# Performance work log

Measured on AMD Instinct MI355X. Metric: run time of the kernel, lower is better.

Reference implementation:

```python
import jax, jax.numpy as jnp
import numpy as np

N, D, H, DH, FF, NE, NNZ = 4096, 128, 2, 64, 256, 2048, 65536
EPS = 1e-5

def layer_norm(x, g, b):
    m = jnp.mean(x, axis=-1, keepdims=True)
    v = jnp.var(x, axis=-1, keepdims=True)
    return (x - m) / jnp.sqrt(v + EPS) * g + b

def setup_inputs() -> dict:
    key = jax.random.key(0)
    ks = jax.random.split(key, 24)
    s = 0.05
    node_idx = jax.random.randint(ks[1], (NNZ,), 0, N)
    he_idx = jax.random.randint(ks[2], (NNZ,), 0, NE)
    return {
        "x": jax.random.normal(ks[0], (N, D), dtype=jnp.float32),
        "edge": jnp.stack([node_idx, he_idx]).astype(jnp.int64),
        "Wq": jax.random.normal(ks[3], (D, D)) * s, "bq": jnp.zeros((D,)),
        "Wk": jax.random.normal(ks[4], (D, D)) * s, "bk": jnp.zeros((D,)),
        "Wv": jax.random.normal(ks[5], (D, D)) * s, "bv": jnp.zeros((D,)),
        "Wo": jax.random.normal(ks[6], (D, D)) * s, "bo": jnp.zeros((D,)),
        "g_ln1": jnp.ones((D,)), "b_ln1": jnp.zeros((D,)),
        "W1": jax.random.normal(ks[7], (D, FF)) * s, "bf1": jnp.zeros((FF,)),
        "W2": jax.random.normal(ks[8], (FF, D)) * s, "bf2": jnp.zeros((D,)),
        "g_ln2": jnp.ones((D,)), "b_ln2": jnp.zeros((D,)),
        "Wh": jax.random.normal(ks[9], (D, D)) * s, "bh": jnp.zeros((D,)),
    }

def reference(x, edge, Wq, bq, Wk, bk, Wv, bv, Wo, bo, g_ln1, b_ln1,
              W1, bf1, W2, bf2, g_ln2, b_ln2, Wh, bh):
    # dropout layers run in eval mode (identity) for a deterministic reference
    def mha_block(h):
        q = (h @ Wq + bq).reshape(N, H, DH)
        k = (h @ Wk + bk).reshape(N, H, DH)
        v = (h @ Wv + bv).reshape(N, H, DH)
        scores = jnp.einsum('nhd,mhd->hnm', q, k) / jnp.sqrt(jnp.float32(DH))
        attn = jax.nn.softmax(scores, axis=-1)            # [H,N,N]
        o = jnp.einsum('hnm,mhd->nhd', attn, v).reshape(N, D)
        return layer_norm(h + o @ Wo + bo, g_ln1, b_ln1)

    def ff_block(h):
        z = jax.nn.sigmoid(h @ W1 + bf1)
        return layer_norm(h + z @ W2 + bf2, g_ln2, b_ln2)

    h = ff_block(mha_block(x))
    h = ff_block(mha_block(h))

    # HypergraphConv: out = D^{-1} H B^{-1} H^T (X Theta) + bias
    node_idx = edge[0]
    he_idx = edge[1]
    xt = h @ Wh                                            # [N,D]
    ones = jnp.ones((NNZ,), dtype=xt.dtype)
    Bdeg = jax.ops.segment_sum(ones, he_idx, num_segments=NE)
    Binv = jnp.where(Bdeg > 0, 1.0 / Bdeg, 0.0)
    Ddeg = jax.ops.segment_sum(ones, node_idx, num_segments=N)
    Dinv = jnp.where(Ddeg > 0, 1.0 / Ddeg, 0.0)
    e = jax.ops.segment_sum(xt[node_idx], he_idx, num_segments=NE) * Binv[:, None]
    out = jax.ops.segment_sum(e[he_idx], node_idx, num_segments=N) * Dinv[:, None] + bh
    return jax.nn.relu(out)
```

## Files before the change

kernel.cpp:

```cpp
#include <hip/hip_runtime.h>
#include <hip/hip_bf16.h>
#include <cstddef>

#define N_NODES 4096
#define DIM     128
#define NHEAD   2
#define DHEAD   64
#define FFDIM   256
#define NEDGE   2048
#define NNZ_E   65536
#define NSPLIT  8

typedef __attribute__((ext_vector_type(8))) short bf16x8;
typedef __attribute__((ext_vector_type(4))) float f32x4;
typedef unsigned short u16;

__device__ __forceinline__ u16 f2b(float f) {
    unsigned u = __float_as_uint(f);
    return (u16)((u + 0x7FFFu + ((u >> 16) & 1u)) >> 16);
}
__device__ __forceinline__ float b2f_bits(u16 h) {
    return __uint_as_float(((unsigned)h) << 16);
}
__device__ __forceinline__ unsigned cvtpk(float a, float b) {
    unsigned r;
    asm("v_cvt_pk_bf16_f32 %0, %1, %2" : "=v"(r) : "v"(a), "v"(b));
    return r;
}

__global__ void prep(const float* __restrict__ x, float* __restrict__ h,
                     u16* __restrict__ hh, u16* __restrict__ hl,
                     const float* W0, const float* W1, const float* W2,
                     const float* W3, const float* W4, const float* W5,
                     const float* W6,
                     u16* P0, u16* P1, u16* P2, u16* P3, u16* P4, u16* P5, u16* P6,
                     const int* __restrict__ edge_raw,
                     int* __restrict__ nidx, int* __restrict__ hidx,
                     int* __restrict__ cnt_e, int* __restrict__ cnt_n) {
    const int bx = blockIdx.x;
    if (bx < 2048) {
        int i = bx * 256 + threadIdx.x;
        float f = x[i];
        h[i] = f;
        u16 hi = f2b(f);
        hh[i] = hi;
        hl[i] = f2b(f - b2f_bits(hi));
        return;
    }
    if (bx >= 2944) {
        __shared__ int is64_s;
        if (threadIdx.x < 64) {
            int v = edge_raw[2 * threadIdx.x + 1];
            unsigned long long bal = __ballot(v != 0);
            if (threadIdx.x == 0) is64_s = (bal == 0ull) ? 1 : 0;
        }
        __syncthreads();
        const int is64 = is64_s;
        int i = (bx - 2944) * 256 + threadIdx.x;
        if (i < NNZ_E) {
            int ni = (is64 ? edge_raw[2 * i]             : edge_raw[i])         & (N_NODES - 1);
            int he = (is64 ? edge_raw[2 * NNZ_E + 2 * i] : edge_raw[NNZ_E + i]) & (NEDGE - 1);
            nidx[i] = ni;
            hidx[i] = he;
            atomicAdd(&cnt_n[ni], 1);
            atomicAdd(&cnt_e[he], 1);
        }
        return;
    }
    const int p = bx - 2048;
    const int sel = p >> 7;
    const float* W; u16* P; int K, NC;
    switch (sel) {
        case 0: W = W0; P = P0; K = 128; NC = 128; break;
        case 1: W = W1; P = P1; K = 128; NC = 128; break;
        case 2: W = W2; P = P2; K = 128; NC = 128; break;
        case 3: W = W3; P = P3; K = 128; NC = 128; break;
        case 4: W = W4; P = P4; K = 128; NC = 128; break;
        case 5: W = W5; P = P5; K = 128; NC = 256; break;
        default: W = W6; P = P6; K = 256; NC = 128; break;
    }
    int i = (p & 127) * 256 + threadIdx.x;
    if (i < K * NC) {
        int k = i / NC, n = i % NC;
        float f = W[i];
        u16 hb = f2b(f);
        size_t o = ((size_t)(k >> 3) * NC + n) * 8 + (k & 7);
        P[o] = hb;
        P[(size_t)K * NC + o] = f2b(f - b2f_bits(hb));
    }
}

__global__ __launch_bounds__(256) void qkv_mfma(const u16* __restrict__ Ah,
                                                const u16* __restrict__ Al,
                                                const u16* __restrict__ Wq,
                                                const u16* __restrict__ Wk,
                                                const u16* __restrict__ Wv,
                                                const float* __restrict__ bq,
                                                const float* __restrict__ bk,
                                                const float* __restrict__ bv,
                                                u16* __restrict__ qb,
                                                u16* __restrict__ kb,
                                                u16* __restrict__ vtb) {
    const int K = 128, NC = 128;
    const int tid = threadIdx.x, w = tid >> 6, lane = tid & 63;
    const int qi = lane & 15, gi = lane >> 4;
    const int row0 = blockIdx.x * 64 + w * 16;
    const int sel = blockIdx.y >> 2;
    const int col0 = (blockIdx.y & 3) * 32;
    const u16* Wp = (sel == 0) ? Wq : (sel == 1) ? Wk : Wv;
    const float* bias = (sel == 0) ? bq : (sel == 1) ? bk : bv;
    const u16* Wlo = Wp + (size_t)K * NC;

    f32x4 acc[2];
    acc[0] = (f32x4){0.f, 0.f, 0.f, 0.f};
    acc[1] = (f32x4){0.f, 0.f, 0.f, 0.f};

#pragma unroll 4
    for (int kc = 0; kc < K / 32; ++kc) {
        const int k0 = kc * 32;
        const size_t ao = (size_t)(row0 + qi) * K + k0 + gi * 8;
        bf16x8 ah = *(const bf16x8*)(Ah + ao);
        bf16x8 al = *(const bf16x8*)(Al + ao);
#pragma unroll
        for (int c = 0; c < 2; ++c) {
            const size_t wo = ((size_t)(k0 / 8 + gi) * NC + col0 + c * 16 + qi) * 8;
            bf16x8 wh = *(const bf16x8*)(Wp + wo);
            bf16x8 wl = *(const bf16x8*)(Wlo + wo);
            acc[c] = __builtin_amdgcn_mfma_f32_16x16x32_bf16(ah, wh, acc[c], 0, 0, 0);
            acc[c] = __builtin_amdgcn_mfma_f32_16x16x32_bf16(al, wh, acc[c], 0, 0, 0);
            acc[c] = __builtin_amdgcn_mfma_f32_16x16x32_bf16(ah, wl, acc[c], 0, 0, 0);
        }
    }

#pragma unroll
    for (int c = 0; c < 2; ++c) {
        const int col = col0 + c * 16 + qi;
        const int hh = col >> 6, d = col & 63;
        float bv_ = bias[col];
        if (sel < 2) {
            u16* dst = (sel == 0) ? qb : kb;
#pragma unroll
            for (int r = 0; r < 4; ++r) {
                const int grow = row0 + gi * 4 + r;
                dst[((size_t)hh * N_NODES + grow) * 64 + d] = f2b(acc[c][r] + bv_);
            }
        } else {
            const int grow0 = row0 + gi * 4;
            uint2 pw;
            pw.x = cvtpk(acc[c][0] + bv_, acc[c][1] + bv_);
            pw.y = cvtpk(acc[c][2] + bv_, acc[c][3] + bv_);
            *(uint2*)&vtb[((size_t)hh * 64 + d) * N_NODES + grow0] = pw;
        }
    }
}

#define ROWP 72
__global__ __launch_bounds__(256) void attn_mfma(const u16* __restrict__ qb,
                                                 const u16* __restrict__ kb,
                                                 const u16* __restrict__ vtb,
                                                 float* __restrict__ op,
                                                 float* __restrict__ mlm,
                                                 float* __restrict__ mll) {
    __shared__ __align__(16) u16 k_s[64 * ROWP];
    __shared__ __align__(16) u16 vt_s[64 * ROWP];
    __shared__ __align__(16) u16 p_s[4][16 * ROWP];
    const int h = blockIdx.y;
    const int s = blockIdx.z;
    const int row0 = blockIdx.x * 64;
    const int tid = threadIdx.x;
    const int w = tid >> 6, lane = tid & 63;
    const int qi = lane & 15, gi = lane >> 4;
    const float CE = 0.18033688011f;
    const float THR = 44.36f;

    const u16* qrow = qb + ((size_t)h * N_NODES + row0 + w * 16 + qi) * 64 + gi * 8;
    bf16x8 qf0 = *(const bf16x8*)qrow;
    bf16x8 qf1 = *(const bf16x8*)(qrow + 32);

    f32x4 oc[4];
#pragma unroll
    for (int i = 0; i < 4; ++i) oc[i] = (f32x4){0.f, 0.f, 0.f, 0.f};
    float m_run = -INFINITY, l_run = 0.f;

    const u16* kbh = kb + (size_t)h * N_NODES * 64;
    const u16* vth = vtb + (size_t)h * 64 * N_NODES;

    for (int kt = s * (N_NODES / 64 / NSPLIT); kt < (s + 1) * (N_NODES / 64 / NSPLIT); ++kt) {
        const u16* ksrc = kbh + kt * 64 * 64;
#pragma unroll
        for (int i = 0; i < 2; ++i) {
            int c = tid + i * 256;
            int r = c >> 3, ss = c & 7;
            *(uint4*)&k_s[r * ROWP + ss * 8]  = *(const uint4*)(ksrc + c * 8);
            *(uint4*)&vt_s[r * ROWP + ss * 8] = *(const uint4*)(vth + (size_t)r * N_NODES + kt * 64 + ss * 8);
        }
        __syncthreads();

        f32x4 sc[4];
#pragma unroll
        for (int t = 0; t < 4; ++t) {
            const u16* krow = &k_s[(t * 16 + qi) * ROWP + gi * 8];
            bf16x8 ka0 = *(const bf16x8*)krow;
            bf16x8 ka1 = *(const bf16x8*)(krow + 32);
            f32x4 z = (f32x4){0.f, 0.f, 0.f, 0.f};
            z = __builtin_amdgcn_mfma_f32_16x16x32_bf16(ka0, qf0, z, 0, 0, 0);
            sc[t] = __builtin_amdgcn_mfma_f32_16x16x32_bf16(ka1, qf1, z, 0, 0, 0);
        }

        float smax = -INFINITY;
#pragma unroll
        for (int t = 0; t < 4; ++t)
            smax = fmaxf(smax, fmaxf(fmaxf(sc[t][0], sc[t][1]), fmaxf(sc[t][2], sc[t][3])));
        smax = fmaxf(smax, __shfl_xor(smax, 16));
        smax = fmaxf(smax, __shfl_xor(smax, 32));

        const bool renew = !__all(smax <= m_run + THR);
        float alpha;
        if (renew) {
            float mn = fmaxf(m_run, smax);
            alpha = exp2f((m_run - mn) * CE);
            m_run = mn;
        }
        float nb = m_run * CE;
        float psum = 0.f;
#pragma unroll
        for (int t = 0; t < 4; ++t) {
            float p0 = exp2f(fmaf(sc[t][0], CE, -nb));
            float p1 = exp2f(fmaf(sc[t][1], CE, -nb));
            float p2 = exp2f(fmaf(sc[t][2], CE, -nb));
            float p3 = exp2f(fmaf(sc[t][3], CE, -nb));
            psum += (p0 + p1) + (p2 + p3);
            uint2 pw;
            pw.x = cvtpk(p0, p1);
            pw.y = cvtpk(p2, p3);
            *(uint2*)&p_s[w][qi * ROWP + t * 16 + gi * 4] = pw;
        }
        psum += __shfl_xor(psum, 16);
        psum += __shfl_xor(psum, 32);

        if (renew) {
            float a0 = __shfl(alpha, gi * 4 + 0);
            float a1 = __shfl(alpha, gi * 4 + 1);
            float a2 = __shfl(alpha, gi * 4 + 2);
            float a3 = __shfl(alpha, gi * 4 + 3);
#pragma unroll
            for (int d = 0; d < 4; ++d) {
                oc[d][0] *= a0; oc[d][1] *= a1; oc[d][2] *= a2; oc[d][3] *= a3;
            }
            l_run = l_run * alpha + psum;
        } else {
            l_run += psum;
        }

        const u16* prow = &p_s[w][qi * ROWP];
        bf16x8 pa0 = *(const bf16x8*)(prow + gi * 8);
        bf16x8 pa1 = *(const bf16x8*)(prow + 32 + gi * 8);
#pragma unroll
        for (int d = 0; d < 4; ++d) {
            const u16* vrow = &vt_s[(d * 16 + qi) * ROWP + gi * 8];
            bf16x8 vb0 = *(const bf16x8*)vrow;
            bf16x8 vb1 = *(const bf16x8*)(vrow + 32);
            oc[d] = __builtin_amdgcn_mfma_f32_16x16x32_bf16(pa0, vb0, oc[d], 0, 0, 0);
            oc[d] = __builtin_amdgcn_mfma_f32_16x16x32_bf16(pa1, vb1, oc[d], 0, 0, 0);
        }
        __syncthreads();
    }

    float* opd = op + (size_t)s * N_NODES * 128;
#pragma unroll
    for (int d = 0; d < 4; ++d) {
        size_t cb = h * 64 + d * 16 + qi;
        opd[(size_t)(row0 + w * 16 + gi * 4 + 0) * 128 + cb] = oc[d][0];
        opd[(size_t)(row0 + w * 16 + gi * 4 + 1) * 128 + cb] = oc[d][1];
        opd[(size_t)(row0 + w * 16 + gi * 4 + 2) * 128 + cb] = oc[d][2];
        opd[(size_t)(row0 + w * 16 + gi * 4 + 3) * 128 + cb] = oc[d][3];
    }
    if (gi == 0) {
        size_t mi = (size_t)s * NHEAD * N_NODES + (size_t)h * N_NODES + row0 + w * 16 + qi;
        mlm[mi] = m_run;
        mll[mi] = l_run;
    }
}

#define ROWA 136
#define ROWZ 264
#define ROWH 132
template<int DO_QKV>
__global__ __launch_bounds__(256) void mega_layer(
        const float* __restrict__ op, const float* __restrict__ mlm,
        const float* __restrict__ mll,
        const u16* __restrict__ wp_o, const float* __restrict__ bo,
        float* __restrict__ h,
        const float* __restrict__ g1, const float* __restrict__ b1,
        const u16* __restrict__ wp_1, const float* __restrict__ bf1,
        const u16* __restrict__ wp_2, const float* __restrict__ bf2,
        const float* __restrict__ g2, const float* __restrict__ b2,
        const u16* __restrict__ wp_q, const u16* __restrict__ wp_k,
        const u16* __restrict__ wp_v,
        const float* __restrict__ bq, const float* __restrict__ bk,
        const float* __restrict__ bv,
        u16* __restrict__ qb, u16* __restrict__ kb, u16* __restrict__ vtb,
        const u16* __restrict__ wp_h, float* __restrict__ xt) {
    __shared__ __align__(16) u16 zbuf[16 * ROWZ * 2];
    __shared__ __align__(16) u16 hp_hi[16 * ROWA];
    __shared__ __align__(16) u16 hp_lo[16 * ROWA];
    __shared__ float hln[16 * ROWH];
    __shared__ float ws_s[NSPLIT][32];
    __shared__ float Linv_s[32];
    __shared__ float wsum[4][16], wsq[4][16];
    const float CE = 0.18033688011f;
    const int tid = threadIdx.x, w = tid >> 6, lane = tid & 63;
    const int qi = lane & 15, gi = lane >> 4;
    const int row0 = blockIdx.x * 16;
    u16* a_hi = zbuf;
    u16* a_lo = zbuf + 16 * ROWA;
    u16* z_hi = zbuf;
    u16* z_lo = zbuf + 16 * ROWZ;

    if (tid < 32) {
        int r = tid >> 1, hd = tid & 1;
        size_t mb = (size_t)hd * N_NODES + row0 + r;
        float m[NSPLIT], l[NSPLIT], mx = -INFINITY;
#pragma unroll
        for (int s = 0; s < NSPLIT; ++s) {
            m[s] = mlm[mb + (size_t)s * NHEAD * N_NODES];
            l[s] = mll[mb + (size_t)s * NHEAD * N_NODES];
            mx = fmaxf(mx, m[s]);
        }
        float L = 0.f;
#pragma unroll
        for (int s = 0; s < NSPLIT; ++s) {
            float ws = exp2f((m[s] - mx) * CE);
            ws_s[s][tid] = ws;
            L += ws * l[s];
        }
        Linv_s[tid] = 1.f / L;
    }
    __syncthreads();

    for (int e = tid; e < 16 * 128; e += 256) {
        int r = e >> 7, c = e & 127, hd = c >> 6;
        size_t idx = (size_t)(row0 + r) * 128 + c;
        float O = 0.f;
#pragma unroll
        for (int s = 0; s < NSPLIT; ++s)
            O += ws_s[s][r * 2 + hd] * op[(size_t)s * N_NODES * 128 + idx];
        float v = O * Linv_s[r * 2 + hd];
        u16 hi = f2b(v);
        a_hi[r * ROWA + c] = hi;
        a_lo[r * ROWA + c] = f2b(v - b2f_bits(hi));
    }
    __syncthreads();

    {
        const u16* Wlo = wp_o + (size_t)128 * 128;
        f32x4 acc[2];
        acc[0] = (f32x4){0.f, 0.f, 0.f, 0.f};
        acc[1] = (f32x4){0.f, 0.f, 0.f, 0.f};
        const int col0 = w * 32;
#pragma unroll
        for (int kc = 0; kc < 4; ++kc) {
            const int k0 = kc * 32;
            bf16x8 ah = *(const bf16x8*)&a_hi[qi * ROWA + k0 + gi * 8];
            bf16x8 al = *(const bf16x8*)&a_lo[qi * ROWA + k0 + gi * 8];
#pragma unroll
            for (int c = 0; c < 2; ++c) {
                const size_t wo = ((size_t)(k0 / 8 + gi) * 128 + col0 + c * 16 + qi) * 8;
                bf16x8 wh = *(const bf16x8*)(wp_o + wo);
                bf16x8 wl = *(const bf16x8*)(Wlo + wo);
                acc[c] = __builtin_amdgcn_mfma_f32_16x16x32_bf16(ah, wh, acc[c], 0, 0, 0);
                acc[c] = __builtin_amdgcn_mfma_f32_16x16x32_bf16(al, wh, acc[c], 0, 0, 0);
                acc[c] = __builtin_amdgcn_mfma_f32_16x16x32_bf16(ah, wl, acc[c], 0, 0, 0);
            }
        }
        float y[2][4], rs[4], rq[4];
#pragma unroll
        for (int r = 0; r < 4; ++r) { rs[r] = 0.f; rq[r] = 0.f; }
#pragma unroll
        for (int c = 0; c < 2; ++c) {
            const int col = col0 + c * 16 + qi;
            float bv = bo[col];
#pragma unroll
            for (int r = 0; r < 4; ++r) {
                float v = acc[c][r] + bv + h[(size_t)(row0 + gi * 4 + r) * 128 + col];
                y[c][r] = v;
                rs[r] += v; rq[r] += v * v;
            }
        }
#pragma unroll
        for (int r = 0; r < 4; ++r)
            for (int msk = 1; msk < 16; msk <<= 1) {
                rs[r] += __shfl_xor(rs[r], msk);
                rq[r] += __shfl_xor(rq[r], msk);
            }
        if (qi == 0) {
#pragma unroll
            for (int r = 0; r < 4; ++r) { wsum[w][gi * 4 + r] = rs[r]; wsq[w][gi * 4 + r] = rq[r]; }
        }
        __syncthreads();
#pragma unroll
        for (int r = 0; r < 4; ++r) {
            const int lr = gi * 4 + r;
            float ts = wsum[0][lr] + wsum[1][lr] + wsum[2][lr] + wsum[3][lr];
            float tq = wsq[0][lr] + wsq[1][lr] + wsq[2][lr] + wsq[3][lr];
            float mean = ts * (1.f / 128.f);
            float var  = tq * (1.f / 128.f) - mean * mean;
            float rstd = rsqrtf(var + 1e-5f);
#pragma unroll
            for (int c = 0; c < 2; ++c) {
                const int col = col0 + c * 16 + qi;
                float yn = (y[c][r] - mean) * rstd * g1[col] + b1[col];
                hln[lr * ROWH + col] = yn;
                u16 hi = f2b(yn);
                hp_hi[lr * ROWA + col] = hi;
                hp_lo[lr * ROWA + col] = f2b(yn - b2f_bits(hi));
            }
        }
    }
    __syncthreads();

    {
        const u16* W1lo = wp_1 + (size_t)128 * 256;
        f32x4 acc1[4];
#pragma unroll
        for (int t = 0; t < 4; ++t) acc1[t] = (f32x4){0.f, 0.f, 0.f, 0.f};
#pragma unroll
        for (int kc = 0; kc < 4; ++kc) {
            const int k0 = kc * 32;
            bf16x8 ah = *(const bf16x8*)&hp_hi[qi * ROWA + k0 + gi * 8];
            bf16x8 al = *(const bf16x8*)&hp_lo[qi * ROWA + k0 + gi * 8];
#pragma unroll
            for (int t = 0; t < 4; ++t) {
                const size_t wo = ((size_t)(k0 / 8 + gi) * 256 + w * 64 + t * 16 + qi) * 8;
                bf16x8 wh = *(const bf16x8*)(wp_1 + wo);
                bf16x8 wl = *(const bf16x8*)(W1lo + wo);
                acc1[t] = __builtin_amdgcn_mfma_f32_16x16x32_bf16(ah, wh, acc1[t], 0, 0, 0);
                acc1[t] = __builtin_amdgcn_mfma_f32_16x16x32_bf16(al, wh, acc1[t], 0, 0, 0);
                acc1[t] = __builtin_amdgcn_mfma_f32_16x16x32_bf16(ah, wl, acc1[t], 0, 0, 0);
            }
        }
        __syncthreads();
#pragma unroll
        for (int t = 0; t < 4; ++t) {
            const int col = w * 64 + t * 16 + qi;
            float bv = bf1[col];
#pragma unroll
            for (int r = 0; r < 4; ++r) {
                float v = acc1[t][r] + bv;
                v = 1.f / (1.f + __expf(-v));
                u16 hi = f2b(v);
                const int zr = gi * 4 + r;
                z_hi[zr * ROWZ + col] = hi;
                z_lo[zr * ROWZ + col] = f2b(v - b2f_bits(hi));
            }
        }
    }
    __syncthreads();

    {
        const u16* W2lo = wp_2 + (size_t)256 * 128;
        f32x4 acc[2];
        acc[0] = (f32x4){0.f, 0.f, 0.f, 0.f};
        acc[1] = (f32x4){0.f, 0.f, 0.f, 0.f};
        const int col0 = w * 32;
#pragma unroll
        for (int kc = 0; kc < 8; ++kc) {
            const int k0 = kc * 32;
            bf16x8 ah = *(const bf16x8*)&z_hi[qi * ROWZ + k0 + gi * 8];
            bf16x8 al = *(const bf16x8*)&z_lo[qi * ROWZ + k0 + gi * 8];
#pragma unroll
            for (int c = 0; c < 2; ++c) {
                const size_t wo = ((size_t)(k0 / 8 + gi) * 128 + col0 + c * 16 + qi) * 8;
                bf16x8 wh = *(const bf16x8*)(wp_2 + wo);
                bf16x8 wl = *(const bf16x8*)(W2lo + wo);
                acc[c] = __builtin_amdgcn_mfma_f32_16x16x32_bf16(ah, wh, acc[c], 0, 0, 0);
                acc[c] = __builtin_amdgcn_mfma_f32_16x16x32_bf16(al, wh, acc[c], 0, 0, 0);
                acc[c] = __builtin_amdgcn_mfma_f32_16x16x32_bf16(ah, wl, acc[c], 0, 0, 0);
            }
        }
        float y[2][4], rs[4], rq[4];
#pragma unroll
        for (int r = 0; r < 4; ++r) { rs[r] = 0.f; rq[r] = 0.f; }
#pragma unroll
        for (int c = 0; c < 2; ++c) {
            const int col = col0 + c * 16 + qi;
            float bv = bf2[col];
#pragma unroll
            for (int r = 0; r < 4; ++r) {
                float v = acc[c][r] + bv + hln[(gi * 4 + r) * ROWH + col];
                y[c][r] = v;
                rs[r] += v; rq[r] += v * v;
            }
        }
#pragma unroll
        for (int r = 0; r < 4; ++r)
            for (int msk = 1; msk < 16; msk <<= 1) {
                rs[r] += __shfl_xor(rs[r], msk);
                rq[r] += __shfl_xor(rq[r], msk);
            }
        if (qi == 0) {
#pragma unroll
            for (int r = 0; r < 4; ++r) { wsum[w][gi * 4 + r] = rs[r]; wsq[w][gi * 4 + r] = rq[r]; }
        }
        __syncthreads();
#pragma unroll
        for (int r = 0; r < 4; ++r) {
            const int lr = gi * 4 + r;
            float ts = wsum[0][lr] + wsum[1][lr] + wsum[2][lr] + wsum[3][lr];
            float tq = wsq[0][lr] + wsq[1][lr] + wsq[2][lr] + wsq[3][lr];
            float mean = ts * (1.f / 128.f);
            float var  = tq * (1.f / 128.f) - mean * mean;
            float rstd = rsqrtf(var + 1e-5f);
#pragma unroll
            for (int c = 0; c < 2; ++c) {
                const int col = col0 + c * 16 + qi;
                float yn = (y[c][r] - mean) * rstd * g2[col] + b2[col];
                if (DO_QKV) h[(size_t)(row0 + lr) * 128 + col] = yn;
                u16 hi = f2b(yn);
                hp_hi[lr * ROWA + col] = hi;
                hp_lo[lr * ROWA + col] = f2b(yn - b2f_bits(hi));
            }
        }
    }

    if (DO_QKV) {
        __syncthreads();
        const int col0 = w * 32;
#pragma unroll
        for (int sel = 0; sel < 3; ++sel) {
            const u16* Wp = (sel == 0) ? wp_q : (sel == 1) ? wp_k : wp_v;
            const float* bias = (sel == 0) ? bq : (sel == 1) ? bk : bv;
            const u16* Wlo = Wp + (size_t)128 * 128;
            f32x4 acc[2];
            acc[0] = (f32x4){0.f, 0.f, 0.f, 0.f};
            acc[1] = (f32x4){0.f, 0.f, 0.f, 0.f};
#pragma unroll
            for (int kc = 0; kc < 4; ++kc) {
                const int k0 = kc * 32;
                bf16x8 ah = *(const bf16x8*)&hp_hi[qi * ROWA + k0 + gi * 8];
                bf16x8 al = *(const bf16x8*)&hp_lo[qi * ROWA + k0 + gi * 8];
#pragma unroll
                for (int c = 0; c < 2; ++c) {
                    const size_t wo = ((size_t)(k0 / 8 + gi) * 128 + col0 + c * 16 + qi) * 8;
                    bf16x8 wh = *(const bf16x8*)(Wp + wo);
                    bf16x8 wl = *(const bf16x8*)(Wlo + wo);
                    acc[c] = __builtin_amdgcn_mfma_f32_16x16x32_bf16(ah, wh, acc[c], 0, 0, 0);
                    acc[c] = __builtin_amdgcn_mfma_f32_16x16x32_bf16(al, wh, acc[c], 0, 0, 0);
                    acc[c] = __builtin_amdgcn_mfma_f32_16x16x32_bf16(ah, wl, acc[c], 0, 0, 0);
                }
            }
#pragma unroll
            for (int c = 0; c < 2; ++c) {
                const int col = col0 + c * 16 + qi;
                const int hh = col >> 6, d = col & 63;
                float bv_ = bias[col];
                if (sel < 2) {
                    u16* dst = (sel == 0) ? qb : kb;
#pragma unroll
                    for (int r = 0; r < 4; ++r) {
                        const int grow = row0 + gi * 4 + r;
                        dst[((size_t)hh * N_NODES + grow) * 64 + d] = f2b(acc[c][r] + bv_);
                    }
                } else {
                    const int grow0 = row0 + gi * 4;
                    uint2 pw;
                    pw.x = cvtpk(acc[c][0] + bv_, acc[c][1] + bv_);
                    pw.y = cvtpk(acc[c][2] + bv_, acc[c][3] + bv_);
                    *(uint2*)&vtb[((size_t)hh * 64 + d) * N_NODES + grow0] = pw;
                }
            }
        }
    } else {
        __syncthreads();
        const u16* Wlo = wp_h + (size_t)128 * 128;
        f32x4 acc[2];
        acc[0] = (f32x4){0.f, 0.f, 0.f, 0.f};
        acc[1] = (f32x4){0.f, 0.f, 0.f, 0.f};
        const int col0 = w * 32;
#pragma unroll
        for (int kc = 0; kc < 4; ++kc) {
            const int k0 = kc * 32;
            bf16x8 ah = *(const bf16x8*)&hp_hi[qi * ROWA + k0 + gi * 8];
            bf16x8 al = *(const bf16x8*)&hp_lo[qi * ROWA + k0 + gi * 8];
#pragma unroll
            for (int c = 0; c < 2; ++c) {
                const size_t wo = ((size_t)(k0 / 8 + gi) * 128 + col0 + c * 16 + qi) * 8;
                bf16x8 wh = *(const bf16x8*)(wp_h + wo);
                bf16x8 wl = *(const bf16x8*)(Wlo + wo);
                acc[c] = __builtin_amdgcn_mfma_f32_16x16x32_bf16(ah, wh, acc[c], 0, 0, 0);
                acc[c] = __builtin_amdgcn_mfma_f32_16x16x32_bf16(al, wh, acc[c], 0, 0, 0);
                acc[c] = __builtin_amdgcn_mfma_f32_16x16x32_bf16(ah, wl, acc[c], 0, 0, 0);
            }
        }
#pragma unroll
        for (int c = 0; c < 2; ++c) {
            const int col = col0 + c * 16 + qi;
#pragma unroll
            for (int r = 0; r < 4; ++r)
                xt[(size_t)(row0 + gi * 4 + r) * 128 + col] = acc[c][r];
        }
    }
}

__global__ __launch_bounds__(1024) void scan_only(const int* __restrict__ cnt_e,
                                                  const int* __restrict__ cnt_n,
                                                  int* __restrict__ off_e,
                                                  int* __restrict__ off_n,
                                                  int* __restrict__ cur_e,
                                                  int* __restrict__ cur_n) {
    __shared__ int s[N_NODES];
    const int he_side = (blockIdx.x == 0);
    const int n = he_side ? NEDGE : N_NODES;
    const int* cnt = he_side ? cnt_e : cnt_n;
    int* off = he_side ? off_e : off_n;
    int* cur = he_side ? cur_e : cur_n;
    for (int i = threadIdx.x; i < n; i += 1024) s[i] = cnt[i];
    __syncthreads();
    for (int st = 1; st < n; st <<= 1) {
        int v[4]; int nj = 0;
        for (int i = threadIdx.x; i < n; i += 1024) v[nj++] = (i >= st) ? s[i - st] : 0;
        __syncthreads();
        nj = 0;
        for (int i = threadIdx.x; i < n; i += 1024) s[i] += v[nj++];
        __syncthreads();
    }
    for (int i = threadIdx.x; i < n; i += 1024) { off[i + 1] = s[i]; cur[i] = 0; }
    if (threadIdx.x == 0) off[0] = 0;
}

__global__ void fill_csr(const int* __restrict__ nidx, const int* __restrict__ hidx,
                         const int* __restrict__ off_e, const int* __restrict__ off_n,
                         int* __restrict__ cur_e, int* __restrict__ cur_n,
                         int* __restrict__ csr_e, int* __restrict__ csr_n) {
    int i = blockIdx.x * 256 + threadIdx.x;
    if (i < NNZ_E) {
        int ni = nidx[i], he = hidx[i];
        int p = atomicAdd(&cur_e[he], 1);
        csr_e[off_e[he] + p] = ni;
        int q = atomicAdd(&cur_n[ni], 1);
        csr_n[off_n[ni] + q] = he;
    }
}

__global__ __launch_bounds__(128) void gather_e(const int* __restrict__ off_e,
                                                const int* __restrict__ csr_e,
                                                const float* __restrict__ xt,
                                                float* __restrict__ e_sc) {
    __shared__ int ms[128];
    const int he = blockIdx.x, d = threadIdx.x;
    const int beg = off_e[he], end = off_e[he + 1];
    float a0 = 0.f, a1 = 0.f, a2 = 0.f, a3 = 0.f;
    for (int c = beg; c < end; c += 128) {
        int nl = min(128, end - c);
        if (d < nl) ms[d] = csr_e[c + d];
        __syncthreads();
        int j = 0;
        for (; j + 3 < nl; j += 4) {
            a0 += xt[(size_t)ms[j]     * 128 + d];
            a1 += xt[(size_t)ms[j + 1] * 128 + d];
            a2 += xt[(size_t)ms[j + 2] * 128 + d];
            a3 += xt[(size_t)ms[j + 3] * 128 + d];
        }
        for (; j < nl; ++j) a0 += xt[(size_t)ms[j] * 128 + d];
        __syncthreads();
    }
    float binv = (end > beg) ? 1.f / (float)(end - beg) : 0.f;
    e_sc[(size_t)he * 128 + d] = ((a0 + a1) + (a2 + a3)) * binv;
}

__global__ __launch_bounds__(128) void gather_n(const int* __restrict__ off_n,
                                                const int* __restrict__ csr_n,
                                                const float* __restrict__ e_sc,
                                                const float* __restrict__ bh,
                                                float* __restrict__ out) {
    __shared__ int ms[128];
    const int nn = blockIdx.x, d = threadIdx.x;
    const int beg = off_n[nn], end = off_n[nn + 1];
    float a0 = 0.f, a1 = 0.f, a2 = 0.f, a3 = 0.f;
    for (int c = beg; c < end; c += 128) {
        int nl = min(128, end - c);
        if (d < nl) ms[d] = csr_n[c + d];
        __syncthreads();
        int j = 0;
        for (; j + 3 < nl; j += 4) {
            a0 += e_sc[(size_t)ms[j]     * 128 + d];
            a1 += e_sc[(size_t)ms[j + 1] * 128 + d];
            a2 += e_sc[(size_t)ms[j + 2] * 128 + d];
            a3 += e_sc[(size_t)ms[j + 3] * 128 + d];
        }
        for (; j < nl; ++j) a0 += e_sc[(size_t)ms[j] * 128 + d];
        __syncthreads();
    }
    float dinv = (end > beg) ? 1.f / (float)(end - beg) : 0.f;
    float v = ((a0 + a1) + (a2 + a3)) * dinv + bh[d];
    out[(size_t)nn * 128 + d] = v > 0.f ? v : 0.f;
}

extern "C" void kernel_launch(void* const* d_in, const int* in_sizes, int n_in,
                              void* d_out, int out_size, void* d_ws, size_t ws_size,
                              hipStream_t stream) {
    (void)in_sizes; (void)n_in; (void)out_size; (void)ws_size;
    const float* x    = (const float*)d_in[0];
    const int*   edge = (const int*)  d_in[1];
    const float* Wq = (const float*)d_in[2];  const float* bq  = (const float*)d_in[3];
    const float* Wk = (const float*)d_in[4];  const float* bk  = (const float*)d_in[5];
    const float* Wv = (const float*)d_in[6];  const float* bv  = (const float*)d_in[7];
    const float* Wo = (const float*)d_in[8];  const float* bo  = (const float*)d_in[9];
    const float* g1 = (const float*)d_in[10]; const float* b1  = (const float*)d_in[11];
    const float* W1 = (const float*)d_in[12]; const float* bf1 = (const float*)d_in[13];
    const float* W2 = (const float*)d_in[14]; const float* bf2 = (const float*)d_in[15];
    const float* g2 = (const float*)d_in[16]; const float* b2  = (const float*)d_in[17];
    const float* Wh = (const float*)d_in[18]; const float* bh  = (const float*)d_in[19];
    float* out = (float*)d_out;

    float* B = (float*)d_ws;
    float* h    = B;
    u16*   h_hi = (u16*)(B + 524288);
    u16*   h_lo = (u16*)(B + 786432);
    u16*   qb   = (u16*)(B + 1048576);
    u16*   kb   = (u16*)(B + 1310720);
    u16*   vtb  = (u16*)(B + 1835008);
    float* op   = B + 2097152;
    float* mlm  = B + 6291456;
    float* mll  = B + 6356992;
    float* xt   = B + 6946816;
    float* e_sc = B + 7471104;
    u16*   wp_q = (u16*)(B + 8519680);
    u16*   wp_k = (u16*)(B + 8536064);
    u16*   wp_v = (u16*)(B + 8552448);
    u16*   wp_o = (u16*)(B + 8568832);
    u16*   wp_h = (u16*)(B + 8585216);
    u16*   wp_1 = (u16*)(B + 8601600);
    u16*   wp_2 = (u16*)(B + 8634368);
    int*   cur_e = (int*)(B + 9328640);
    int*   cur_n = (int*)(B + 9330688);
    int*   off_e = (int*)(B + 9334784);
    int*   off_n = (int*)(B + 9336840);
    int*   csr_e = (int*)(B + 9340944);
    int*   csr_n = (int*)(B + 9406480);
    int*   cnt_e = (int*)(B + 9472016);
    int*   cnt_n = (int*)(B + 9474064);
    int*   nidx  = (int*)(B + 9478160);
    int*   hidx  = (int*)(B + 9543696);

    hipMemsetAsync(cnt_e, 0, (NEDGE + N_NODES) * sizeof(int), stream);

    prep<<<3200, 256, 0, stream>>>(x, h, h_hi, h_lo,
                                   Wq, Wk, Wv, Wo, Wh, W1, W2,
                                   wp_q, wp_k, wp_v, wp_o, wp_h, wp_1, wp_2,
                                   edge, nidx, hidx, cnt_e, cnt_n);

    qkv_mfma<<<dim3(64, 12), 256, 0, stream>>>(h_hi, h_lo, wp_q, wp_k, wp_v,
                                               bq, bk, bv, qb, kb, vtb);
    attn_mfma<<<dim3(N_NODES / 64, NHEAD, NSPLIT), 256, 0, stream>>>(qb, kb, vtb, op, mlm, mll);
    mega_layer<1><<<N_NODES / 16, 256, 0, stream>>>(op, mlm, mll, wp_o, bo, h, g1, b1,
                                                    wp_1, bf1, wp_2, bf2, g2, b2,
                                                    wp_q, wp_k, wp_v, bq, bk, bv,
                                                    qb, kb, vtb, wp_h, xt);
    attn_mfma<<<dim3(N_NODES / 64, NHEAD, NSPLIT), 256, 0, stream>>>(qb, kb, vtb, op, mlm, mll);
    mega_layer<0><<<N_NODES / 16, 256, 0, stream>>>(op, mlm, mll, wp_o, bo, h, g1, b1,
                                                    wp_1, bf1, wp_2, bf2, g2, b2,
                                                    nullptr, nullptr, nullptr,
                                                    nullptr, nullptr, nullptr,
                                                    nullptr, nullptr, nullptr,
                                                    wp_h, xt);

    scan_only<<<2, 1024, 0, stream>>>(cnt_e, cnt_n, off_e, off_n, cur_e, cur_n);
    fill_csr<<<NNZ_E / 256, 256, 0, stream>>>(nidx, hidx, off_e, off_n, cur_e, cur_n, csr_e, csr_n);
    gather_e<<<NEDGE, 128, 0, stream>>>(off_e, csr_e, xt, e_sc);
    gather_n<<<N_NODES, 128, 0, stream>>>(off_n, csr_n, e_sc, bh, out);
}
```

Before: 255.6 us.

## Double block size to 512 threads in attention and fused layer kernels

The attention kernel now uses 8 waves per block covering 128 query rows, so each K/V tile loaded into shared memory is reused by twice as many query rows. The fused layer kernel moves to 8 waves per 16-row tile, each wave computing 16 output columns instead of 32, and the LayerNorm partial sums are reduced across 8 waves. The aim is to cut per-block K/V staging traffic and raise per-block parallelism. The cost is fewer attention blocks in the grid and more cross-wave reduction and barrier overhead in the layer kernel.

Result: faster. 234.2 us (-8.3%).

```diff
diff --git a/kernel.cpp b/kernel.cpp
--- a/kernel.cpp
+++ b/kernel.cpp
@@ -155,7 +155,7 @@
 }
 
 #define ROWP 72
-__global__ __launch_bounds__(256) void attn_mfma(const u16* __restrict__ qb,
+__global__ __launch_bounds__(512) void attn_mfma(const u16* __restrict__ qb,
                                                  const u16* __restrict__ kb,
                                                  const u16* __restrict__ vtb,
                                                  float* __restrict__ op,
@@ -163,10 +163,10 @@
                                                  float* __restrict__ mll) {
     __shared__ __align__(16) u16 k_s[64 * ROWP];
     __shared__ __align__(16) u16 vt_s[64 * ROWP];
-    __shared__ __align__(16) u16 p_s[4][16 * ROWP];
+    __shared__ __align__(16) u16 p_s[8][16 * ROWP];
     const int h = blockIdx.y;
     const int s = blockIdx.z;
-    const int row0 = blockIdx.x * 64;
+    const int row0 = blockIdx.x * 128;
     const int tid = threadIdx.x;
     const int w = tid >> 6, lane = tid & 63;
     const int qi = lane & 15, gi = lane >> 4;
@@ -187,11 +187,9 @@
 
     for (int kt = s * (N_NODES / 64 / NSPLIT); kt < (s + 1) * (N_NODES / 64 / NSPLIT); ++kt) {
         const u16* ksrc = kbh + kt * 64 * 64;
-#pragma unroll
-        for (int i = 0; i < 2; ++i) {
-            int c = tid + i * 256;
-            int r = c >> 3, ss = c & 7;
-            *(uint4*)&k_s[r * ROWP + ss * 8]  = *(const uint4*)(ksrc + c * 8);
+        {
+            int r = tid >> 3, ss = tid & 7;
+            *(uint4*)&k_s[r * ROWP + ss * 8]  = *(const uint4*)(ksrc + tid * 8);
             *(uint4*)&vt_s[r * ROWP + ss * 8] = *(const uint4*)(vth + (size_t)r * N_NODES + kt * 64 + ss * 8);
         }
         __syncthreads();
@@ -286,7 +284,7 @@
 #define ROWZ 264
 #define ROWH 132
 template<int DO_QKV>
-__global__ __launch_bounds__(256) void mega_layer(
+__global__ __launch_bounds__(512) void mega_layer(
         const float* __restrict__ op, const float* __restrict__ mlm,
         const float* __restrict__ mll,
         const u16* __restrict__ wp_o, const float* __restrict__ bo,
@@ -307,7 +305,7 @@
     __shared__ float hln[16 * ROWH];
     __shared__ float ws_s[NSPLIT][32];
     __shared__ float Linv_s[32];
-    __shared__ float wsum[4][16], wsq[4][16];
+    __shared__ float wsum[8][16], wsq[8][16];
     const float CE = 0.18033688011f;
     const int tid = threadIdx.x, w = tid >> 6, lane = tid & 63;
     const int qi = lane & 15, gi = lane >> 4;
@@ -338,7 +336,7 @@
     }
     __syncthreads();
 
-    for (int e = tid; e < 16 * 128; e += 256) {
+    for (int e = tid; e < 16 * 128; e += 512) {
         int r = e >> 7, c = e & 127, hd = c >> 6;
         size_t idx = (size_t)(row0 + r) * 128 + c;
         float O = 0.f;
@@ -354,38 +352,28 @@
 
     {
         const u16* Wlo = wp_o + (size_t)128 * 128;
-        f32x4 acc[2];
-        acc[0] = (f32x4){0.f, 0.f, 0.f, 0.f};
-        acc[1] = (f32x4){0.f, 0.f, 0.f, 0.f};
-        const int col0 = w * 32;
+        f32x4 acc = (f32x4){0.f, 0.f, 0.f, 0.f};
+        const int col0 = w * 16;
 #pragma unroll
         for (int kc = 0; kc < 4; ++kc) {
             const int k0 = kc * 32;
             bf16x8 ah = *(const bf16x8*)&a_hi[qi * ROWA + k0 + gi * 8];
             bf16x8 al = *(const bf16x8*)&a_lo[qi * ROWA + k0 + gi * 8];
-#pragma unroll
-            for (int c = 0; c < 2; ++c) {
-                const size_t wo = ((size_t)(k0 / 8 + gi) * 128 + col0 + c * 16 + qi) * 8;
-                bf16x8 wh = *(const bf16x8*)(wp_o + wo);
-                bf16x8 wl = *(const bf16x8*)(Wlo + wo);
-                acc[c] = __builtin_amdgcn_mfma_f32_16x16x32_bf16(ah, wh, acc[c], 0, 0, 0);
-                acc[c] = __builtin_amdgcn_mfma_f32_16x16x32_bf16(al, wh, acc[c], 0, 0, 0);
-                acc[c] = __builtin_amdgcn_mfma_f32_16x16x32_bf16(ah, wl, acc[c], 0, 0, 0);
-            }
-        }
-        float y[2][4], rs[4], rq[4];
-#pragma unroll
-        for (int r = 0; r < 4; ++r) { rs[r] = 0.f; rq[r] = 0.f; }
-#pragma unroll
-        for (int c = 0; c < 2; ++c) {
-            const int col = col0 + c * 16 + qi;
-            float bv = bo[col];
-#pragma unroll
-            for (int r = 0; r < 4; ++r) {
-                float v = acc[c][r] + bv + h[(size_t)(row0 + gi * 4 + r) * 128 + col];
-                y[c][r] = v;
-                rs[r] += v; rq[r] += v * v;
-            }
+            const size_t wo = ((size_t)(k0 / 8 + gi) * 128 + col0 + qi) * 8;
+            bf16x8 wh = *(const bf16x8*)(wp_o + wo);
+            bf16x8 wl = *(const bf16x8*)(Wlo + wo);
+            acc = __builtin_amdgcn_mfma_f32_16x16x32_bf16(ah, wh, acc, 0, 0, 0);
+            acc = __builtin_amdgcn_mfma_f32_16x16x32_bf16(al, wh, acc, 0, 0, 0);
+            acc = __builtin_amdgcn_mfma_f32_16x16x32_bf16(ah, wl, acc, 0, 0, 0);
+        }
+        float y[4], rs[4], rq[4];
+        const int col = col0 + qi;
+        float bvv = bo[col];
+#pragma unroll
+        for (int r = 0; r < 4; ++r) {
+            float v = acc[r] + bvv + h[(size_t)(row0 + gi * 4 + r) * 128 + col];
+            y[r] = v;
+            rs[r] = v; rq[r] = v * v;
         }
 #pragma unroll
         for (int r = 0; r < 4; ++r)
@@ -401,37 +389,34 @@
 #pragma unroll
         for (int r = 0; r < 4; ++r) {
             const int lr = gi * 4 + r;
-            float ts = wsum[0][lr] + wsum[1][lr] + wsum[2][lr] + wsum[3][lr];
-            float tq = wsq[0][lr] + wsq[1][lr] + wsq[2][lr] + wsq[3][lr];
+            float ts = 0.f, tq = 0.f;
+#pragma unroll
+            for (int ww = 0; ww < 8; ++ww) { ts += wsum[ww][lr]; tq += wsq[ww][lr]; }
             float mean = ts * (1.f / 128.f);
             float var  = tq * (1.f / 128.f) - mean * mean;
             float rstd = rsqrtf(var + 1e-5f);
-#pragma unroll
-            for (int c = 0; c < 2; ++c) {
-                const int col = col0 + c * 16 + qi;
-                float yn = (y[c][r] - mean) * rstd * g1[col] + b1[col];
-                hln[lr * ROWH + col] = yn;
-                u16 hi = f2b(yn);
-                hp_hi[lr * ROWA + col] = hi;
-                hp_lo[lr * ROWA + col] = f2b(yn - b2f_bits(hi));
-            }
+            float yn = (y[r] - mean) * rstd * g1[col] + b1[col];
+            hln[lr * ROWH + col] = yn;
+            u16 hi = f2b(yn);
+            hp_hi[lr * ROWA + col] = hi;
+            hp_lo[lr * ROWA + col] = f2b(yn - b2f_bits(hi));
         }
     }
     __syncthreads();
 
     {
         const u16* W1lo = wp_1 + (size_t)128 * 256;
-        f32x4 acc1[4];
-#pragma unroll
-        for (int t = 0; t < 4; ++t) acc1[t] = (f32x4){0.f, 0.f, 0.f, 0.f};
+        f32x4 acc1[2];
+#pragma unroll
+        for (int t = 0; t < 2; ++t) acc1[t] = (f32x4){0.f, 0.f, 0.f, 0.f};
 #pragma unroll
         for (int kc = 0; kc < 4; ++kc) {
             const int k0 = kc * 32;
             bf16x8 ah = *(const bf16x8*)&hp_hi[qi * ROWA + k0 + gi * 8];
             bf16x8 al = *(const bf16x8*)&hp_lo[qi * ROWA + k0 + gi * 8];
 #pragma unroll
-            for (int t = 0; t < 4; ++t) {
-                const size_t wo = ((size_t)(k0 / 8 + gi) * 256 + w * 64 + t * 16 + qi) * 8;
+            for (int t = 0; t < 2; ++t) {
+                const size_t wo = ((size_t)(k0 / 8 + gi) * 256 + w * 32 + t * 16 + qi) * 8;
                 bf16x8 wh = *(const bf16x8*)(wp_1 + wo);
                 bf16x8 wl = *(const bf16x8*)(W1lo + wo);
                 acc1[t] = __builtin_amdgcn_mfma_f32_16x16x32_bf16(ah, wh, acc1[t], 0, 0, 0);
@@ -441,12 +426,12 @@
         }
         __syncthreads();
 #pragma unroll
-        for (int t = 0; t < 4; ++t) {
-            const int col = w * 64 + t * 16 + qi;
-            float bv = bf1[col];
+        for (int t = 0; t < 2; ++t) {
+            const int col = w * 32 + t * 16 + qi;
+            float bvv = bf1[col];
 #pragma unroll
             for (int r = 0; r < 4; ++r) {
-                float v = acc1[t][r] + bv;
+                float v = acc1[t][r] + bvv;
                 v = 1.f / (1.f + __expf(-v));
                 u16 hi = f2b(v);
                 const int zr = gi * 4 + r;
@@ -459,38 +444,28 @@
 
     {
         const u16* W2lo = wp_2 + (size_t)256 * 128;
-        f32x4 acc[2];
-        acc[0] = (f32x4){0.f, 0.f, 0.f, 0.f};
-        acc[1] = (f32x4){0.f, 0.f, 0.f, 0.f};
-        const int col0 = w * 32;
+        f32x4 acc = (f32x4){0.f, 0.f, 0.f, 0.f};
+        const int col0 = w * 16;
 #pragma unroll
         for (int kc = 0; kc < 8; ++kc) {
             const int k0 = kc * 32;
             bf16x8 ah = *(const bf16x8*)&z_hi[qi * ROWZ + k0 + gi * 8];
             bf16x8 al = *(const bf16x8*)&z_lo[qi * ROWZ + k0 + gi * 8];
-#pragma unroll
-            for (int c = 0; c < 2; ++c) {
-                const size_t wo = ((size_t)(k0 / 8 + gi) * 128 + col0 + c * 16 + qi) * 8;
-                bf16x8 wh = *(const bf16x8*)(wp_2 + wo);
-                bf16x8 wl = *(const bf16x8*)(W2lo + wo);
-                acc[c] = __builtin_amdgcn_mfma_f32_16x16x32_bf16(ah, wh, acc[c], 0, 0, 0);
-                acc[c] = __builtin_amdgcn_mfma_f32_16x16x32_bf16(al, wh, acc[c], 0, 0, 0);
-                acc[c] = __builtin_amdgcn_mfma_f32_16x16x32_bf16(ah, wl, acc[c], 0, 0, 0);
-            }
-        }
-        float y[2][4], rs[4], rq[4];
-#pragma unroll
-        for (int r = 0; r < 4; ++r) { rs[r] = 0.f; rq[r] = 0.f; }
-#pragma unroll
-        for (int c = 0; c < 2; ++c) {
-            const int col = col0 + c * 16 + qi;
-            float bv = bf2[col];
-#pragma unroll
-            for (int r = 0; r < 4; ++r) {
-                float v = acc[c][r] + bv + hln[(gi * 4 + r) * ROWH + col];
-                y[c][r] = v;
-                rs[r] += v; rq[r] += v * v;
-            }
+            const size_t wo = ((size_t)(k0 / 8 + gi) * 128 + col0 + qi) * 8;
+            bf16x8 wh = *(const bf16x8*)(wp_2 + wo);
+            bf16x8 wl = *(const bf16x8*)(W2lo + wo);
+            acc = __builtin_amdgcn_mfma_f32_16x16x32_bf16(ah, wh, acc, 0, 0, 0);
+            acc = __builtin_amdgcn_mfma_f32_16x16x32_bf16(al, wh, acc, 0, 0, 0);
+            acc = __builtin_amdgcn_mfma_f32_16x16x32_bf16(ah, wl, acc, 0, 0, 0);
+        }
+        float y[4], rs[4], rq[4];
+        const int col = col0 + qi;
+        float bvv = bf2[col];
+#pragma unroll
+        for (int r = 0; r < 4; ++r) {
+            float v = acc[r] + bvv + hln[(gi * 4 + r) * ROWH + col];
+            y[r] = v;
+            rs[r] = v; rq[r] = v * v;
         }
 #pragma unroll
         for (int r = 0; r < 4; ++r)
@@ -506,99 +481,80 @@
 #pragma unroll
         for (int r = 0; r < 4; ++r) {
             const int lr = gi * 4 + r;
-            float ts = wsum[0][lr] + wsum[1][lr] + wsum[2][lr] + wsum[3][lr];
-            float tq = wsq[0][lr] + wsq[1][lr] + wsq[2][lr] + wsq[3][lr];
+            float ts = 0.f, tq = 0.f;
+#pragma unroll
+            for (int ww = 0; ww < 8; ++ww) { ts += wsum[ww][lr]; tq += wsq[ww][lr]; }
             float mean = ts * (1.f / 128.f);
             float var  = tq * (1.f / 128.f) - mean * mean;
             float rstd = rsqrtf(var + 1e-5f);
-#pragma unroll
-            for (int c = 0; c < 2; ++c) {
-                const int col = col0 + c * 16 + qi;
-                float yn = (y[c][r] - mean) * rstd * g2[col] + b2[col];
-                if (DO_QKV) h[(size_t)(row0 + lr) * 128 + col] = yn;
-                u16 hi = f2b(yn);
-                hp_hi[lr * ROWA + col] = hi;
-                hp_lo[lr * ROWA + col] = f2b(yn - b2f_bits(hi));
-            }
+            float yn = (y[r] - mean) * rstd * g2[col] + b2[col];
+            if (DO_QKV) h[(size_t)(row0 + lr) * 128 + col] = yn;
+            u16 hi = f2b(yn);
+            hp_hi[lr * ROWA + col] = hi;
+            hp_lo[lr * ROWA + col] = f2b(yn - b2f_bits(hi));
         }
     }
 
     if (DO_QKV) {
         __syncthreads();
-        const int col0 = w * 32;
+        const int col0 = w * 16;
 #pragma unroll
         for (int sel = 0; sel < 3; ++sel) {
             const u16* Wp = (sel == 0) ? wp_q : (sel == 1) ? wp_k : wp_v;
             const float* bias = (sel == 0) ? bq : (sel == 1) ? bk : bv;
             const u16* Wlo = Wp + (size_t)128 * 128;
-            f32x4 acc[2];
-            acc[0] = (f32x4){0.f, 0.f, 0.f, 0.f};
-            acc[1] = (f32x4){0.f, 0.f, 0.f, 0.f};
+            f32x4 acc = (f32x4){0.f, 0.f, 0.f, 0.f};
 #pragma unroll
             for (int kc = 0; kc < 4; ++kc) {
                 const int k0 = kc * 32;
                 bf16x8 ah = *(const bf16x8*)&hp_hi[qi * ROWA + k0 + gi * 8];
                 bf16x8 al = *(const bf16x8*)&hp_lo[qi * ROWA + k0 + gi * 8];
-#pragma unroll
-                for (int c = 0; c < 2; ++c) {
-                    const size_t wo = ((size_t)(k0 / 8 + gi) * 128 + col0 + c * 16 + qi) * 8;
-                    bf16x8 wh = *(const bf16x8*)(Wp + wo);
-                    bf16x8 wl = *(const bf16x8*)(Wlo + wo);
-                    acc[c] = __builtin_amdgcn_mfma_f32_16x16x32_bf16(ah, wh, acc[c], 0, 0, 0);
-                    acc[c] = __builtin_amdgcn_mfma_f32_16x16x32_bf16(al, wh, acc[c], 0, 0, 0);
-                    acc[c] = __builtin_amdgcn_mfma_f32_16x16x32_bf16(ah, wl, acc[c], 0, 0, 0);
+                const size_t wo = ((size_t)(k0 / 8 + gi) * 128 + col0 + qi) * 8;
+                bf16x8 wh = *(const bf16x8*)(Wp + wo);
+                bf16x8 wl = *(const bf16x8*)(Wlo + wo);
+                acc = __builtin_amdgcn_mfma_f32_16x16x32_bf16(ah, wh, acc, 0, 0, 0);
+                acc = __builtin_amdgcn_mfma_f32_16x16x32_bf16(al, wh, acc, 0, 0, 0);
+                acc = __builtin_amdgcn_mfma_f32_16x16x32_bf16(ah, wl, acc, 0, 0, 0);
+            }
+            const int col = col0 + qi;
+            const int hh = col >> 6, d = col & 63;
+            float bv_ = bias[col];
+            if (sel < 2) {
+                u16* dst = (sel == 0) ? qb : kb;
+#pragma unroll
+                for (int r = 0; r < 4; ++r) {
+                    const int grow = row0 + gi * 4 + r;
+                    dst[((size_t)hh * N_NODES + grow) * 64 + d] = f2b(acc[r] + bv_);
                 }
+            } else {
+                const int grow0 = row0 + gi * 4;
+                uint2 pw;
+                pw.x = cvtpk(acc[0] + bv_, acc[1] + bv_);
+                pw.y = cvtpk(acc[2] + bv_, acc[3] + bv_);
+                *(uint2*)&vtb[((size_t)hh * 64 + d) * N_NODES + grow0] = pw;
             }
-#pragma unroll
-            for (int c = 0; c < 2; ++c) {
-                const int col = col0 + c * 16 + qi;
-                const int hh = col >> 6, d = col & 63;
-                float bv_ = bias[col];
-                if (sel < 2) {
-                    u16* dst = (sel == 0) ? qb : kb;
-#pragma unroll
-                    for (int r = 0; r < 4; ++r) {
-                        const int grow = row0 + gi * 4 + r;
-                        dst[((size_t)hh * N_NODES + grow) * 64 + d] = f2b(acc[c][r] + bv_);
-                    }
-                } else {
-                    const int grow0 = row0 + gi * 4;
-                    uint2 pw;
-                    pw.x = cvtpk(acc[c][0] + bv_, acc[c][1] + bv_);
-                    pw.y = cvtpk(acc[c][2] + bv_, acc[c][3] + bv_);
-                    *(uint2*)&vtb[((size_t)hh * 64 + d) * N_NODES + grow0] = pw;
-                }
-            }
         }
     } else {
         __syncthreads();
         const u16* Wlo = wp_h + (size_t)128 * 128;
-        f32x4 acc[2];
-        acc[0] = (f32x4){0.f, 0.f, 0.f, 0.f};
-        acc[1] = (f32x4){0.f, 0.f, 0.f, 0.f};
-        const int col0 = w * 32;
+        f32x4 acc = (f32x4){0.f, 0.f, 0.f, 0.f};
+        const int col0 = w * 16;
 #pragma unroll
         for (int kc = 0; kc < 4; ++kc) {
             const int k0 = kc * 32;
             bf16x8 ah = *(const bf16x8*)&hp_hi[qi * ROWA + k0 + gi * 8];
             bf16x8 al = *(const bf16x8*)&hp_lo[qi * ROWA + k0 + gi * 8];
-#pragma unroll
-            for (int c = 0; c < 2; ++c) {
-                const size_t wo = ((size_t)(k0 / 8 + gi) * 128 + col0 + c * 16 + qi) * 8;
-                bf16x8 wh = *(const bf16x8*)(wp_h + wo);
-                bf16x8 wl = *(const bf16x8*)(Wlo + wo);
-                acc[c] = __builtin_amdgcn_mfma_f32_16x16x32_bf16(ah, wh, acc[c], 0, 0, 0);
-                acc[c] = __builtin_amdgcn_mfma_f32_16x16x32_bf16(al, wh, acc[c], 0, 0, 0);
-                acc[c] = __builtin_amdgcn_mfma_f32_16x16x32_bf16(ah, wl, acc[c], 0, 0, 0);
-            }
-        }
-#pragma unroll
-        for (int c = 0; c < 2; ++c) {
-            const int col = col0 + c * 16 + qi;
-#pragma unroll
-            for (int r = 0; r < 4; ++r)
-                xt[(size_t)(row0 + gi * 4 + r) * 128 + col] = acc[c][r];
-        }
+            const size_t wo = ((size_t)(k0 / 8 + gi) * 128 + col0 + qi) * 8;
+            bf16x8 wh = *(const bf16x8*)(wp_h + wo);
+            bf16x8 wl = *(const bf16x8*)(Wlo + wo);
+            acc = __builtin_amdgcn_mfma_f32_16x16x32_bf16(ah, wh, acc, 0, 0, 0);
+            acc = __builtin_amdgcn_mfma_f32_16x16x32_bf16(al, wh, acc, 0, 0, 0);
+            acc = __builtin_amdgcn_mfma_f32_16x16x32_bf16(ah, wl, acc, 0, 0, 0);
+        }
+        const int col = col0 + qi;
+#pragma unroll
+        for (int r = 0; r < 4; ++r)
+            xt[(size_t)(row0 + gi * 4 + r) * 128 + col] = acc[r];
     }
 }
 
@@ -752,13 +708,13 @@
 
     qkv_mfma<<<dim3(64, 12), 256, 0, stream>>>(h_hi, h_lo, wp_q, wp_k, wp_v,
                                                bq, bk, bv, qb, kb, vtb);
-    attn_mfma<<<dim3(N_NODES / 64, NHEAD, NSPLIT), 256, 0, stream>>>(qb, kb, vtb, op, mlm, mll);
-    mega_layer<1><<<N_NODES / 16, 256, 0, stream>>>(op, mlm, mll, wp_o, bo, h, g1, b1,
+    attn_mfma<<<dim3(N_NODES / 128, NHEAD, NSPLIT), 512, 0, stream>>>(qb, kb, vtb, op, mlm, mll);
+    mega_layer<1><<<N_NODES / 16, 512, 0, stream>>>(op, mlm, mll, wp_o, bo, h, g1, b1,
                                                     wp_1, bf1, wp_2, bf2, g2, b2,
                                                     wp_q, wp_k, wp_v, bq, bk, bv,
                                                     qb, kb, vtb, wp_h, xt);
-    attn_mfma<<<dim3(N_NODES / 64, NHEAD, NSPLIT), 256, 0, stream>>>(qb, kb, vtb, op, mlm, mll);
-    mega_layer<0><<<N_NODES / 16, 256, 0, stream>>>(op, mlm, mll, wp_o, bo, h, g1, b1,
+    attn_mfma<<<dim3(N_NODES / 128, NHEAD, NSPLIT), 512, 0, stream>>>(qb, kb, vtb, op, mlm, mll);
+    mega_layer<0><<<N_NODES / 16, 512, 0, stream>>>(op, mlm, mll, wp_o, bo, h, g1, b1,
                                                     wp_1, bf1, wp_2, bf2, g2, b2,
                                                     nullptr, nullptr, nullptr,
                                                     nullptr, nullptr, nullptr,
```
